# Kernel optimization log

Hardware: AMD Instinct MI355X
Metric: run time of the kernel (lower is better)

## Reference

```python
import jax, jax.numpy as jnp
import numpy as np

D = 512      # units / model dim
H = 8        # num_heads
K = 512      # key_dim (= units in this module)
B = 8
T = 512      # decoder length
S = 512      # encoder length
EPS = 1e-3   # Keras LayerNormalization default epsilon


def _layernorm(x, g, b):
    mu = jnp.mean(x, axis=-1, keepdims=True)
    var = jnp.mean(jnp.square(x - mu), axis=-1, keepdims=True)
    return (x - mu) * jax.lax.rsqrt(var + EPS) * g + b


def _mha(q_in, kv_in, wq, bq, wk, bk, wv, bv, wo, bo, causal):
    # q_in: [B,Tq,D], kv_in: [B,Tk,D]; wq/wk/wv: [D,H,K]; wo: [H,K,D]
    q = jnp.einsum('btd,dhk->bthk', q_in, wq) + bq
    k = jnp.einsum('bsd,dhk->bshk', kv_in, wk) + bk
    v = jnp.einsum('bsd,dhk->bshk', kv_in, wv) + bv
    scores = jnp.einsum('bqhk,bshk->bhqs', q, k) / jnp.sqrt(jnp.float32(K))
    if causal:
        Tq, Tk = q.shape[1], k.shape[1]
        mask = jnp.tril(jnp.ones((Tq, Tk), dtype=bool))
        scores = jnp.where(mask[None, None], scores, jnp.finfo(scores.dtype).min)
    attn = jax.nn.softmax(scores, axis=-1)
    out = jnp.einsum('bhqs,bshk->bqhk', attn, v)
    return jnp.einsum('bqhk,hkd->bqd', out, wo) + bo


def setup_inputs() -> dict:
    key = jax.random.key(0)
    ks = jax.random.split(key, 32)
    sc = 0.02
    d = {
        'in_seq': jax.random.normal(ks[0], (B, S, D), jnp.float32),
        'out_seq': jax.random.normal(ks[1], (B, T, D), jnp.float32),
    }
    i = 2
    for pfx in ('sa', 'ca'):
        d[pfx + '_wq'] = jax.random.normal(ks[i], (D, H, K)) * sc; i += 1
        d[pfx + '_bq'] = jnp.zeros((H, K))
        d[pfx + '_wk'] = jax.random.normal(ks[i], (D, H, K)) * sc; i += 1
        d[pfx + '_bk'] = jnp.zeros((H, K))
        d[pfx + '_wv'] = jax.random.normal(ks[i], (D, H, K)) * sc; i += 1
        d[pfx + '_bv'] = jnp.zeros((H, K))
        d[pfx + '_wo'] = jax.random.normal(ks[i], (H, K, D)) * sc; i += 1
        d[pfx + '_bo'] = jnp.zeros((D,))
        d[pfx + '_lng'] = jnp.ones((D,))
        d[pfx + '_lnb'] = jnp.zeros((D,))
    d['ff_w1'] = jax.random.normal(ks[i], (D, 2 * D)) * sc; i += 1
    d['ff_b1'] = jnp.zeros((2 * D,))
    d['ff_w2'] = jax.random.normal(ks[i], (2 * D, D)) * sc; i += 1
    d['ff_b2'] = jnp.zeros((D,))
    d['ff_lng'] = jnp.ones((D,))
    d['ff_lnb'] = jnp.zeros((D,))
    return d


def reference(in_seq, out_seq,
              sa_wq, sa_bq, sa_wk, sa_bk, sa_wv, sa_bv, sa_wo, sa_bo, sa_lng, sa_lnb,
              ca_wq, ca_bq, ca_wk, ca_bk, ca_wv, ca_bv, ca_wo, ca_bo, ca_lng, ca_lnb,
              ff_w1, ff_b1, ff_w2, ff_b2, ff_lng, ff_lnb):
    # causal self-attention + add + LN
    x = out_seq
    a = _mha(x, x, sa_wq, sa_bq, sa_wk, sa_bk, sa_wv, sa_bv, sa_wo, sa_bo, causal=True)
    x = _layernorm(x + a, sa_lng, sa_lnb)
    # cross-attention + add + LN
    a = _mha(x, in_seq, ca_wq, ca_bq, ca_wk, ca_bk, ca_wv, ca_bv, ca_wo, ca_bo, causal=False)
    x = _layernorm(x + a, ca_lng, ca_lnb)
    # FFN: Dense(2D, gelu) -> Dense(D) (dropout inactive at inference) + add + LN
    h = jax.nn.gelu(x @ ff_w1 + ff_b1, approximate=False)
    x = _layernorm(x + (h @ ff_w2 + ff_b2), ff_lng, ff_lnb)
    return x
```

## Files before the change

### kernel.cpp

```cpp
#include <hip/hip_runtime.h>
#include <math.h>

#define DEV __device__ __forceinline__

typedef __bf16 bf16x8 __attribute__((ext_vector_type(8)));
typedef float f32x4 __attribute__((ext_vector_type(4)));
typedef unsigned short u16x8 __attribute__((ext_vector_type(8)));

typedef const __attribute__((address_space(1))) void gv_t;
typedef __attribute__((address_space(3))) void lv_t;

DEV unsigned short f2bf(float f){
  unsigned int u = __float_as_uint(f);
  u += 0x7fffu + ((u >> 16) & 1u);
  return (unsigned short)(u >> 16);
}
DEV float bf2f(unsigned short u){ return __uint_as_float((unsigned)u << 16); }

DEV void gload16(const void* g, void* l){
  __builtin_amdgcn_global_load_lds((gv_t*)g, (lv_t*)l, 16, 0, 0);
}

DEV void xcd_decode(int& bx, int& by, int& bz){
  const int gx = gridDim.x, gy = gridDim.y;
  const int nwg = gx * gy * gridDim.z;
  int lin = blockIdx.x + gx*(blockIdx.y + gy*blockIdx.z);
  if ((nwg & 7) == 0) lin = (lin & 7)*(nwg >> 3) + (lin >> 3);
  bx = lin % gx; const int t = lin / gx;
  by = t % gy;  bz = t / gy;
}

struct Proj3 {
  const unsigned short* A[3];
  const unsigned short* B[3];
  unsigned short*       C[3];
  const float*          bias[3];
};

__global__ __launch_bounds__(512, 2)
void qkv256(Proj3 pr)
{
  __shared__ unsigned short Ab[2][2][8192];
  __shared__ unsigned short Bb[2][2][8192];

  int bxi, byi, bzi; xcd_decode(bxi, byi, bzi);
  const int m0 = byi*256, n0 = bxi*256;
  const unsigned short* A = pr.A[bzi];
  const unsigned short* B = pr.B[bzi];
  unsigned short*       C = pr.C[bzi];
  const float*       bias = pr.bias[bzi];

  const int tid = threadIdx.x, lane = tid & 63, w = tid >> 6;
  const int wr = w >> 2, wc = w & 3;
  const int l15 = lane & 15, l4 = lane >> 4;

  const int r8  = tid >> 3;
  const int sc8 = ((tid & 7) ^ (r8 & 7)) * 8;

  auto stageA = [&](int buf, int half, int kt){
    #pragma unroll
    for (int j = 0; j < 2; j++){
      const int lr = j*64 + r8;
      gload16(A + (size_t)(m0 + half*128 + lr)*512 + kt + sc8,
              &Ab[buf][half][j*4096 + tid*8]);
    }
  };
  auto stageB = [&](int buf, int half, int kt){
    #pragma unroll
    for (int j = 0; j < 2; j++){
      const int lr = j*64 + r8;
      gload16(B + (size_t)(n0 + half*128 + lr)*512 + kt + sc8,
              &Bb[buf][half][j*4096 + tid*8]);
    }
  };

  f32x4 acc[8][4] = {};

  stageB(0,0,0); stageB(0,1,0);
  stageA(0,0,0); stageA(0,1,0);
  stageA(1,0,64); stageA(1,1,64);
  stageB(1,0,64); stageB(1,1,64);
  asm volatile("s_waitcnt vmcnt(8)" ::: "memory");
  __builtin_amdgcn_s_barrier();
  __builtin_amdgcn_sched_barrier(0);

  const int nt = 8;
  for (int Q = 0; Q < nt; Q++){
    const int cur = Q & 1;
    if (Q > 0){
      if (Q + 1 < nt) asm volatile("s_waitcnt vmcnt(4)" ::: "memory");
      else            asm volatile("s_waitcnt vmcnt(0)" ::: "memory");
      __builtin_amdgcn_s_barrier();
      __builtin_amdgcn_sched_barrier(0);
    }
    bf16x8 bfr[4][2];
    #pragma unroll
    for (int s = 0; s < 4; s++){
      if (s == 0){
        #pragma unroll
        for (int fc = 0; fc < 4; fc++){
          const int R = wc*64 + fc*16 + l15;
          const int hb = R >> 7, lr = R & 127;
          #pragma unroll
          for (int kc = 0; kc < 2; kc++){
            const int cc = (kc*32 + l4*8) ^ ((lr & 7) * 8);
            bfr[fc][kc] = *(const bf16x8*)&Bb[cur][hb][lr*64 + cc];
          }
        }
      }
      bf16x8 ar[2][2];
      #pragma unroll
      for (int f = 0; f < 2; f++){
        const int lr = (s*2 + f)*16 + l15;
        #pragma unroll
        for (int kc = 0; kc < 2; kc++){
          const int cc = (kc*32 + l4*8) ^ ((lr & 7) * 8);
          ar[f][kc] = *(const bf16x8*)&Ab[cur][wr][lr*64 + cc];
        }
      }
      if (s == 0 && Q >= 1 && Q + 1 < nt) stageA(cur ^ 1, 0, (Q+1)*64);
      if (s == 1 && Q >= 1 && Q + 1 < nt) stageA(cur ^ 1, 1, (Q+1)*64);
      if (s == 2 && Q + 2 < nt)           stageB(cur,     0, (Q+2)*64);
      if (s == 3 && Q + 2 < nt)           stageB(cur,     1, (Q+2)*64);

      asm volatile("s_waitcnt lgkmcnt(0)" ::: "memory");
      __builtin_amdgcn_sched_barrier(0);
      __builtin_amdgcn_s_setprio(1);
      #pragma unroll
      for (int f = 0; f < 2; f++)
        #pragma unroll
        for (int fc = 0; fc < 4; fc++)
          #pragma unroll
          for (int kc = 0; kc < 2; kc++)
            acc[s*2+f][fc] = __builtin_amdgcn_mfma_f32_16x16x32_bf16(
                ar[f][kc], bfr[fc][kc], acc[s*2+f][fc], 0, 0, 0);
      __builtin_amdgcn_s_setprio(0);
      __builtin_amdgcn_s_barrier();
      __builtin_amdgcn_sched_barrier(0);
    }
  }

  if (bzi != 2){
    #pragma unroll
    for (int fr = 0; fr < 8; fr++){
      const int mb = m0 + wr*128 + fr*16 + l4*4;
      #pragma unroll
      for (int fc = 0; fc < 4; fc++){
        const int n = n0 + wc*64 + fc*16 + l15;
        const float bv = bias[n];
        #pragma unroll
        for (int r = 0; r < 4; r++)
          C[(size_t)(mb + r)*4096 + n] = f2bf(acc[fr][fc][r] + bv);
      }
    }
  } else {
    unsigned short* vt = C + ((size_t)((n0 >> 9)*8 + (m0 >> 9)))*262144;
    #pragma unroll
    for (int fr = 0; fr < 8; fr++){
      const int mb = m0 + wr*128 + fr*16 + l4*4;
      #pragma unroll
      for (int fc = 0; fc < 4; fc++){
        const int nl = (n0 & 256) + wc*64 + fc*16 + l15;
        #pragma unroll
        for (int r = 0; r < 4; r++){
          const int m = mb + r;
          const float bv = bias[m];
          vt[(size_t)((m0 & 256) + (m - m0))*512 + nl] = f2bf(acc[fr][fc][r] + bv);
        }
      }
    }
  }
}

template<int CMODE, int CSK>
__global__ __launch_bounds__(512, 2)
void gemm256(const unsigned short* __restrict__ A, const unsigned short* __restrict__ B,
             void* __restrict__ C, const float* __restrict__ bias,
             int M, int N, int K, int lda, int ldb, int ldc,
             size_t aOffH, size_t aOffB, size_t bOffH, size_t bOffB,
             size_t cOffH, size_t cOffB)
{
  __shared__ unsigned short Ab[2][2][8192];
  __shared__ unsigned short Bb[2][2][8192];

  int bxi, byi, bzi; xcd_decode(bxi, byi, bzi);
  const int m0 = byi*256, n0 = bxi*256;
  if (CSK == 1 && n0 > m0 + 255) return;

  const int z = bzi, bb = z >> 3, hh = z & 7;
  A += (size_t)bb*aOffB + (size_t)hh*aOffH;
  B += (size_t)bb*bOffB + (size_t)hh*bOffH;
  const size_t coff = (size_t)bb*cOffB + (size_t)hh*cOffH;

  const int tid = threadIdx.x, lane = tid & 63, w = tid >> 6;
  const int wr = w >> 2, wc = w & 3;
  const int l15 = lane & 15, l4 = lane >> 4;

  int Keff = K;
  if (CSK == 2) Keff = (m0 + 256 < K) ? (m0 + 256) : K;
  const int nt = Keff >> 6;

  const int r8  = tid >> 3;
  const int sc8 = ((tid & 7) ^ (r8 & 7)) * 8;

  auto stageA = [&](int buf, int half, int kt){
    #pragma unroll
    for (int j = 0; j < 2; j++){
      const int lr = j*64 + r8;
      gload16(A + (size_t)(m0 + half*128 + lr)*lda + kt + sc8,
              &Ab[buf][half][j*4096 + tid*8]);
    }
  };
  auto stageB = [&](int buf, int half, int kt){
    #pragma unroll
    for (int j = 0; j < 2; j++){
      const int lr = j*64 + r8;
      gload16(B + (size_t)(n0 + half*128 + lr)*ldb + kt + sc8,
              &Bb[buf][half][j*4096 + tid*8]);
    }
  };

  f32x4 acc[8][4] = {};

  stageB(0,0,0); stageB(0,1,0);
  stageA(0,0,0); stageA(0,1,0);
  if (nt > 1){
    stageA(1,0,64); stageA(1,1,64);
    stageB(1,0,64); stageB(1,1,64);
    asm volatile("s_waitcnt vmcnt(8)" ::: "memory");
  } else {
    asm volatile("s_waitcnt vmcnt(0)" ::: "memory");
  }
  __builtin_amdgcn_s_barrier();
  __builtin_amdgcn_sched_barrier(0);

  for (int Q = 0; Q < nt; Q++){
    const int cur = Q & 1;
    if (Q > 0){
      if (Q + 1 < nt) asm volatile("s_waitcnt vmcnt(4)" ::: "memory");
      else            asm volatile("s_waitcnt vmcnt(0)" ::: "memory");
      __builtin_amdgcn_s_barrier();
      __builtin_amdgcn_sched_barrier(0);
    }
    bf16x8 bfr[4][2];
    #pragma unroll
    for (int s = 0; s < 4; s++){
      if (s == 0){
        #pragma unroll
        for (int fc = 0; fc < 4; fc++){
          const int R = wc*64 + fc*16 + l15;
          const int hb = R >> 7, lr = R & 127;
          #pragma unroll
          for (int kc = 0; kc < 2; kc++){
            const int cc = (kc*32 + l4*8) ^ ((lr & 7) * 8);
            bfr[fc][kc] = *(const bf16x8*)&Bb[cur][hb][lr*64 + cc];
          }
        }
      }
      bf16x8 ar[2][2];
      #pragma unroll
      for (int f = 0; f < 2; f++){
        const int lr = (s*2 + f)*16 + l15;
        #pragma unroll
        for (int kc = 0; kc < 2; kc++){
          const int cc = (kc*32 + l4*8) ^ ((lr & 7) * 8);
          ar[f][kc] = *(const bf16x8*)&Ab[cur][wr][lr*64 + cc];
        }
      }
      if (s == 0 && Q >= 1 && Q + 1 < nt) stageA(cur ^ 1, 0, (Q+1)*64);
      if (s == 1 && Q >= 1 && Q + 1 < nt) stageA(cur ^ 1, 1, (Q+1)*64);
      if (s == 2 && Q + 2 < nt)           stageB(cur,     0, (Q+2)*64);
      if (s == 3 && Q + 2 < nt)           stageB(cur,     1, (Q+2)*64);

      asm volatile("s_waitcnt lgkmcnt(0)" ::: "memory");
      __builtin_amdgcn_sched_barrier(0);
      __builtin_amdgcn_s_setprio(1);
      #pragma unroll
      for (int f = 0; f < 2; f++)
        #pragma unroll
        for (int fc = 0; fc < 4; fc++)
          #pragma unroll
          for (int kc = 0; kc < 2; kc++)
            acc[s*2+f][fc] = __builtin_amdgcn_mfma_f32_16x16x32_bf16(
                ar[f][kc], bfr[fc][kc], acc[s*2+f][fc], 0, 0, 0);
      __builtin_amdgcn_s_setprio(0);
      __builtin_amdgcn_s_barrier();
      __builtin_amdgcn_sched_barrier(0);
    }
  }

  #pragma unroll
  for (int fr = 0; fr < 8; fr++){
    const int mb = m0 + wr*128 + fr*16 + l4*4;
    #pragma unroll
    for (int fc = 0; fc < 4; fc++){
      const int n = n0 + wc*64 + fc*16 + l15;
      const float bv = bias ? bias[n] : 0.0f;
      #pragma unroll
      for (int r = 0; r < 4; r++){
        const float v = acc[fr][fc][r] + bv;
        if (CMODE == 0) ((float*)C)[coff + (size_t)(mb + r)*ldc + n] = v;
        else            ((unsigned short*)C)[coff + (size_t)(mb + r)*ldc + n] = f2bf(v);
      }
    }
  }
}

template<int CMODE>
__global__ __launch_bounds__(256, 2)
void gemm_bt(const unsigned short* __restrict__ A, const unsigned short* __restrict__ B,
             void* __restrict__ C, const float* __restrict__ bias,
             int M, int N, int K, int lda, int ldb, int ldc,
             size_t aOffZ, size_t bOffZ, size_t cOffZ)
{
  __shared__ unsigned short Ab[2][8192];
  __shared__ unsigned short Bb[2][8192];

  int bxi, byi, bzi; xcd_decode(bxi, byi, bzi);
  const int m0 = byi*128, n0 = bxi*128;
  A += (size_t)bzi*aOffZ;
  B += (size_t)bzi*bOffZ;
  const size_t coff = (size_t)bzi*cOffZ;

  const int tid = threadIdx.x, lane = tid & 63, w = tid >> 6;
  const int wr = w >> 1, wc = w & 1;
  const int l15 = lane & 15, l4 = lane >> 4;
  const int nt = K >> 6;

  const int r8  = tid >> 3;
  const int sc8 = ((tid & 7) ^ (r8 & 7)) * 8;

  auto stage = [&](int buf, int kt){
    #pragma unroll
    for (int j = 0; j < 4; j++){
      gload16(A + (size_t)(m0 + j*32 + r8)*lda + kt + sc8, &Ab[buf][j*2048 + tid*8]);
      gload16(B + (size_t)(n0 + j*32 + r8)*ldb + kt + sc8, &Bb[buf][j*2048 + tid*8]);
    }
  };

  f32x4 acc[4][4] = {};

  stage(0, 0);
  __syncthreads();
  for (int t = 0; t < nt; t++){
    const int cur = t & 1;
    if (t + 1 < nt) stage(cur ^ 1, (t+1)*64);

    bf16x8 af[4][2], bfr[4][2];
    #pragma unroll
    for (int i = 0; i < 4; i++){
      const int Ra = wr*64 + i*16 + l15;
      const int Rb = wc*64 + i*16 + l15;
      #pragma unroll
      for (int kc = 0; kc < 2; kc++){
        const int ca = (kc*32 + l4*8) ^ ((Ra & 7) * 8);
        const int cb = (kc*32 + l4*8) ^ ((Rb & 7) * 8);
        af[i][kc]  = *(const bf16x8*)&Ab[cur][Ra*64 + ca];
        bfr[i][kc] = *(const bf16x8*)&Bb[cur][Rb*64 + cb];
      }
    }
    #pragma unroll
    for (int i = 0; i < 4; i++)
      #pragma unroll
      for (int jj = 0; jj < 4; jj++)
        #pragma unroll
        for (int kc = 0; kc < 2; kc++)
          acc[i][jj] = __builtin_amdgcn_mfma_f32_16x16x32_bf16(
              af[i][kc], bfr[jj][kc], acc[i][jj], 0, 0, 0);
    __syncthreads();
  }

  #pragma unroll
  for (int i = 0; i < 4; i++){
    const int mbase = m0 + wr*64 + i*16 + l4*4;
    #pragma unroll
    for (int jj = 0; jj < 4; jj++){
      const int n = n0 + wc*64 + jj*16 + l15;
      const float bv = bias ? bias[n] : 0.0f;
      #pragma unroll
      for (int r = 0; r < 4; r++){
        const int m = mbase + r;
        float v = acc[i][jj][r] + bv;
        if (CMODE == 0){
          ((float*)C)[coff + (size_t)m*ldc + n] = v;
        } else if (CMODE == 1){
          ((unsigned short*)C)[coff + (size_t)m*ldc + n] = f2bf(v);
        } else {
          v = 0.5f * v * (1.0f + erff(v * 0.70710678118654752f));
          ((unsigned short*)C)[coff + (size_t)m*ldc + n] = f2bf(v);
        }
      }
    }
  }
}

__global__ __launch_bounds__(256)
void gelu_reduce2(const unsigned short* __restrict__ p, size_t pstride,
                  const float* __restrict__ bias, unsigned short* __restrict__ out)
{
  const size_t i = ((size_t)blockIdx.x*256 + threadIdx.x)*8;
  const int nb = (int)(i & 1023);
  u16x8 a = *(const u16x8*)(p + i);
  u16x8 b = *(const u16x8*)(p + pstride + i);
  u16x8 o;
  #pragma unroll
  for (int j = 0; j < 8; j++){
    float v = bf2f(a[j]) + bf2f(b[j]) + bias[nb + j];
    v = 0.5f * v * (1.0f + erff(v * 0.70710678118654752f));
    o[j] = f2bf(v);
  }
  *(u16x8*)(out + i) = o;
}

template<int CAUSAL>
__global__ __launch_bounds__(256)
void softmax_rows(unsigned short* __restrict__ scores)
{
  const int row  = blockIdx.x*4 + (threadIdx.x >> 6);
  const int lane = threadIdx.x & 63;
  const int q = row & 511;
  unsigned short* srow = scores + (size_t)row*512;
  u16x8 sv = *(const u16x8*)(srow + lane*8);
  float s[8]; float m = -1e30f;
  #pragma unroll
  for (int i = 0; i < 8; i++){
    const int col = lane*8 + i;
    float v = bf2f(sv[i]) * 0.044194173824159216f;
    if (CAUSAL && col > q) v = -1e30f;
    s[i] = v; m = fmaxf(m, v);
  }
  #pragma unroll
  for (int o = 32; o; o >>= 1) m = fmaxf(m, __shfl_xor(m, o));
  float p[8], sum = 0.f;
  #pragma unroll
  for (int i = 0; i < 8; i++){
    float e = __expf(s[i] - m);
    if (CAUSAL && (lane*8 + i) > q) e = 0.f;
    p[i] = e; sum += e;
  }
  #pragma unroll
  for (int o = 32; o; o >>= 1) sum += __shfl_xor(sum, o);
  const float inv = 1.0f / sum;
  u16x8 pv;
  #pragma unroll
  for (int i = 0; i < 8; i++) pv[i] = f2bf(p[i] * inv);
  *(u16x8*)(srow + lane*8) = pv;
}

template<int WRITE_BF, int ND, int BFP>
__global__ __launch_bounds__(256)
void ln_rows(const float* __restrict__ x, const void* __restrict__ dbase,
             size_t dstride, const float* __restrict__ bias,
             const float* __restrict__ g, const float* __restrict__ bta,
             float* __restrict__ xo, unsigned short* __restrict__ xb)
{
  const int row = blockIdx.x*4 + (threadIdx.x >> 6);
  const int lane = threadIdx.x & 63;
  const float* xr = x + (size_t)row*512;
  float v[8];
  #pragma unroll
  for (int i = 0; i < 8; i++){
    const int c = lane*8 + i;
    v[i] = xr[c] + (bias ? bias[c] : 0.0f);
  }
  #pragma unroll
  for (int p = 0; p < ND; p++){
    if (BFP){
      const unsigned short* db = (const unsigned short*)dbase;
      u16x8 dv = *(const u16x8*)(db + p*dstride + (size_t)row*512 + lane*8);
      #pragma unroll
      for (int i = 0; i < 8; i++) v[i] += bf2f(dv[i]);
    } else {
      const float* db = (const float*)dbase;
      #pragma unroll
      for (int i = 0; i < 8; i++) v[i] += db[p*dstride + (size_t)row*512 + lane*8 + i];
    }
  }
  float sum = 0.f;
  #pragma unroll
  for (int i = 0; i < 8; i++) sum += v[i];
  #pragma unroll
  for (int o = 32; o; o >>= 1) sum += __shfl_xor(sum, o);
  const float mean = sum * (1.0f/512.0f);
  float s2 = 0.f;
  #pragma unroll
  for (int i = 0; i < 8; i++){ const float t = v[i] - mean; s2 += t*t; }
  #pragma unroll
  for (int o = 32; o; o >>= 1) s2 += __shfl_xor(s2, o);
  const float inv = rsqrtf(s2 * (1.0f/512.0f) + 1e-3f);
  #pragma unroll
  for (int i = 0; i < 8; i++){
    const int c = lane*8 + i;
    const float y = (v[i] - mean)*inv*g[c] + bta[c];
    xo[(size_t)row*512 + c] = y;
    if (WRITE_BF) xb[(size_t)row*512 + c] = f2bf(y);
  }
}

struct Cast2 { const float* s[2]; unsigned short* d[2]; };

__global__ __launch_bounds__(256)
void cast_bf16_k2(Cast2 a, int n)
{
  const int z = blockIdx.y;
  const int i = (blockIdx.x*256 + threadIdx.x)*4;
  if (i < n){
    const float4 v = *(const float4*)(a.s[z] + i);
    uint2 o;
    o.x = (unsigned)f2bf(v.x) | ((unsigned)f2bf(v.y) << 16);
    o.y = (unsigned)f2bf(v.z) | ((unsigned)f2bf(v.w) << 16);
    *(uint2*)(a.d[z] + i) = o;
  }
}

struct TC8 { const float* s[8]; unsigned short* d[8]; };

__global__ __launch_bounds__(256)
void transpose_cast8(TC8 a, int R, int C)
{
  __shared__ float tile[32][33];
  const int z = blockIdx.z;
  const float* src = a.s[z];
  unsigned short* dst = a.d[z];
  const int bx = blockIdx.x*32, by = blockIdx.y*32;
  const int tx = threadIdx.x & 31, ty = threadIdx.x >> 5;
  #pragma unroll
  for (int i = 0; i < 32; i += 8) tile[ty + i][tx] = src[(size_t)(by + ty + i)*C + bx + tx];
  __syncthreads();
  #pragma unroll
  for (int i = 0; i < 32; i += 8) dst[(size_t)(bx + ty + i)*R + by + tx] = f2bf(tile[tx][ty + i]);
}

extern "C" void kernel_launch(void* const* d_in, const int* in_sizes, int n_in,
                              void* d_out, int out_size, void* d_ws, size_t ws_size,
                              hipStream_t stream)
{
  (void)in_sizes; (void)n_in; (void)out_size; (void)ws_size;

  const float* in_seq  = (const float*)d_in[0];
  const float* out_seq = (const float*)d_in[1];
  const float* sa_wq = (const float*)d_in[2];  const float* sa_bq = (const float*)d_in[3];
  const float* sa_wk = (const float*)d_in[4];  const float* sa_bk = (const float*)d_in[5];
  const float* sa_wv = (const float*)d_in[6];  const float* sa_bv = (const float*)d_in[7];
  const float* sa_wo = (const float*)d_in[8];  const float* sa_bo = (const float*)d_in[9];
  const float* sa_lng = (const float*)d_in[10]; const float* sa_lnb = (const float*)d_in[11];
  const float* ca_wq = (const float*)d_in[12]; const float* ca_bq = (const float*)d_in[13];
  const float* ca_wk = (const float*)d_in[14]; const float* ca_bk = (const float*)d_in[15];
  const float* ca_wv = (const float*)d_in[16]; const float* ca_bv = (const float*)d_in[17];
  const float* ca_wo = (const float*)d_in[18]; const float* ca_bo = (const float*)d_in[19];
  const float* ca_lng = (const float*)d_in[20]; const float* ca_lnb = (const float*)d_in[21];
  const float* ff_w1 = (const float*)d_in[22]; const float* ff_b1 = (const float*)d_in[23];
  const float* ff_w2 = (const float*)d_in[24]; const float* ff_b2 = (const float*)d_in[25];
  const float* ff_lng = (const float*)d_in[26]; const float* ff_lnb = (const float*)d_in[27];

  char* ws = (char*)d_ws;
  size_t off = 0;
  auto alloc = [&](size_t bytes){ char* p = ws + off; off += (bytes + 255) & ~(size_t)255; return p; };

  unsigned short* wT[8];
  for (int i = 0; i < 8; i++) wT[i] = (unsigned short*)alloc(4096ULL*512*2);
  unsigned short* w1T  = (unsigned short*)alloc(1024ULL*512*2);
  unsigned short* w2T  = (unsigned short*)alloc(512ULL*1024*2);
  unsigned short* xbf  = (unsigned short*)alloc(4096ULL*512*2);
  unsigned short* inbf = (unsigned short*)alloc(4096ULL*512*2);
  unsigned short* qb   = (unsigned short*)alloc(4096ULL*4096*2);
  unsigned short* kb   = (unsigned short*)alloc(4096ULL*4096*2);
  unsigned short* vT   = (unsigned short*)alloc(64ULL*512*512*2);
  unsigned short* scb  = (unsigned short*)alloc(64ULL*512*512*2);
  float*          xcur = (float*)alloc(4096ULL*512*4);

  unsigned short* part = scb;
  const size_t PART_STRIDE = 2097152;
  const size_t FF1_STRIDE = 4194304;

  Cast2 c2{{out_seq, in_seq}, {xbf, inbf}};
  cast_bf16_k2<<<dim3(2048,2), 256, 0, stream>>>(c2, 4096*512);

  TC8 tqkv{{sa_wq, sa_wk, sa_wv, ca_wq, ca_wk, ca_wv, nullptr, nullptr},
           {wT[0], wT[1], wT[2], wT[4], wT[5], wT[6], nullptr, nullptr}};
  transpose_cast8<<<dim3(128,16,6), 256, 0, stream>>>(tqkv, 512, 4096);
  TC8 two{{sa_wo, ca_wo, nullptr,nullptr,nullptr,nullptr,nullptr,nullptr},
          {wT[3], wT[7], nullptr,nullptr,nullptr,nullptr,nullptr,nullptr}};
  transpose_cast8<<<dim3(16,128,2), 256, 0, stream>>>(two, 4096, 512);
  TC8 tw1{{ff_w1, nullptr,nullptr,nullptr,nullptr,nullptr,nullptr,nullptr},
          {w1T, nullptr,nullptr,nullptr,nullptr,nullptr,nullptr,nullptr}};
  transpose_cast8<<<dim3(32,16,1), 256, 0, stream>>>(tw1, 512, 1024);
  TC8 tw2{{ff_w2, nullptr,nullptr,nullptr,nullptr,nullptr,nullptr,nullptr},
          {w2T, nullptr,nullptr,nullptr,nullptr,nullptr,nullptr,nullptr}};
  transpose_cast8<<<dim3(16,32,1), 256, 0, stream>>>(tw2, 1024, 512);

  #define G256(MODE, CSK, Apt, Bpt, Cpt, BIAS, M, N, K, LDA, LDB, LDC, Z, aH, aB, bH, bB, cH, cB) \
    gemm256<MODE, CSK><<<dim3((N)/256,(M)/256,(Z)), 512, 0, stream>>>( \
      (const unsigned short*)(Apt), (const unsigned short*)(Bpt), (void*)(Cpt), BIAS, \
      M, N, K, LDA, LDB, LDC, aH, aB, bH, bB, cH, cB)

  Proj3 saP{{xbf, xbf, wT[2]}, {wT[0], wT[1], xbf}, {qb, kb, vT}, {sa_bq, sa_bk, sa_bv}};
  qkv256<<<dim3(16,16,3), 512, 0, stream>>>(saP);
  G256(1, 1, qb, kb, scb, nullptr, 512, 512, 512, 4096, 4096, 512, 64,
       512, 2097152, 512, 2097152, 262144, 2097152);
  softmax_rows<1><<<8192, 256, 0, stream>>>(scb);
  G256(1, 2, scb, vT, kb, nullptr, 512, 512, 512, 512, 512, 4096, 64,
       262144, 2097152, 262144, 2097152, 512, 2097152);
  G256(1, 0, kb, wT[3], part, nullptr, 4096, 512, 512, 4096, 4096, 512, 8,
       512, 0, 512, 0, PART_STRIDE, 0);
  ln_rows<1, 8, 1><<<1024, 256, 0, stream>>>(out_seq, part, PART_STRIDE,
                                             sa_bo, sa_lng, sa_lnb, xcur, xbf);

  Proj3 caP{{xbf, inbf, wT[6]}, {wT[4], wT[5], inbf}, {qb, kb, vT}, {ca_bq, ca_bk, ca_bv}};
  qkv256<<<dim3(16,16,3), 512, 0, stream>>>(caP);
  G256(1, 0, qb, kb, scb, nullptr, 512, 512, 512, 4096, 4096, 512, 64,
       512, 2097152, 512, 2097152, 262144, 2097152);
  softmax_rows<0><<<8192, 256, 0, stream>>>(scb);
  G256(1, 0, scb, vT, kb, nullptr, 512, 512, 512, 512, 512, 4096, 64,
       262144, 2097152, 262144, 2097152, 512, 2097152);
  G256(1, 0, kb, wT[7], part, nullptr, 4096, 512, 512, 4096, 4096, 512, 8,
       512, 0, 512, 0, PART_STRIDE, 0);
  ln_rows<1, 8, 1><<<1024, 256, 0, stream>>>(xcur, part, PART_STRIDE,
                                             ca_bo, ca_lng, ca_lnb, xcur, xbf);

  gemm_bt<1><<<dim3(8,32,2), 256, 0, stream>>>(
      xbf, w1T, (void*)part, nullptr, 4096, 1024, 256, 512, 512, 1024,
      256, 256, FF1_STRIDE);
  gelu_reduce2<<<2048, 256, 0, stream>>>(part, FF1_STRIDE, ff_b1, qb);
  G256(1, 0, qb, w2T, part, nullptr, 4096, 512, 128, 1024, 1024, 512, 8,
       128, 0, 128, 0, PART_STRIDE, 0);
  ln_rows<0, 8, 1><<<1024, 256, 0, stream>>>(xcur, part, PART_STRIDE,
                                             ff_b2, ff_lng, ff_lnb, (float*)d_out, nullptr);

  #undef G256
}
```

Before: 417.1 us.

## Merge weight transpose launches, drop fp32 residual buffer, skip masked causal loads

Folds the four weight transpose-cast launches into one flat-grid kernel that uses a per-tile table. The fp32 residual buffer xcur is removed, so layernorm now reads and writes only the bf16 activation, which cuts memory traffic and lowers the residual to bf16 precision. The causal softmax no longer loads score chunks that lie entirely above the diagonal. The bf16 residual adds rounding error to the layer output.

```diff
diff --git a/kernel.cpp b/kernel.cpp
--- a/kernel.cpp
+++ b/kernel.cpp
@@ -420,7 +420,8 @@
   const int lane = threadIdx.x & 63;
   const int q = row & 511;
   unsigned short* srow = scores + (size_t)row*512;
-  u16x8 sv = *(const u16x8*)(srow + lane*8);
+  u16x8 sv = {};
+  if (!CAUSAL || lane*8 <= q) sv = *(const u16x8*)(srow + lane*8);
   float s[8]; float m = -1e30f;
   #pragma unroll
   for (int i = 0; i < 8; i++){
@@ -447,34 +448,32 @@
   *(u16x8*)(srow + lane*8) = pv;
 }
 
-template<int WRITE_BF, int ND, int BFP>
+template<int XF32, int OUTF32, int ND>
 __global__ __launch_bounds__(256)
-void ln_rows(const float* __restrict__ x, const void* __restrict__ dbase,
+void ln_rows(const void* __restrict__ x, const unsigned short* __restrict__ dbase,
              size_t dstride, const float* __restrict__ bias,
              const float* __restrict__ g, const float* __restrict__ bta,
-             float* __restrict__ xo, unsigned short* __restrict__ xb)
+             void* __restrict__ out)
 {
   const int row = blockIdx.x*4 + (threadIdx.x >> 6);
   const int lane = threadIdx.x & 63;
-  const float* xr = x + (size_t)row*512;
   float v[8];
-  #pragma unroll
-  for (int i = 0; i < 8; i++){
-    const int c = lane*8 + i;
-    v[i] = xr[c] + (bias ? bias[c] : 0.0f);
-  }
+  if (XF32){
+    const float* xr = (const float*)x + (size_t)row*512 + lane*8;
+    #pragma unroll
+    for (int i = 0; i < 8; i++) v[i] = xr[i];
+  } else {
+    u16x8 xv = *(const u16x8*)((const unsigned short*)x + (size_t)row*512 + lane*8);
+    #pragma unroll
+    for (int i = 0; i < 8; i++) v[i] = bf2f(xv[i]);
+  }
+  #pragma unroll
+  for (int i = 0; i < 8; i++) v[i] += bias ? bias[lane*8 + i] : 0.0f;
   #pragma unroll
   for (int p = 0; p < ND; p++){
-    if (BFP){
-      const unsigned short* db = (const unsigned short*)dbase;
-      u16x8 dv = *(const u16x8*)(db + p*dstride + (size_t)row*512 + lane*8);
-      #pragma unroll
-      for (int i = 0; i < 8; i++) v[i] += bf2f(dv[i]);
-    } else {
-      const float* db = (const float*)dbase;
-      #pragma unroll
-      for (int i = 0; i < 8; i++) v[i] += db[p*dstride + (size_t)row*512 + lane*8 + i];
-    }
+    u16x8 dv = *(const u16x8*)(dbase + p*dstride + (size_t)row*512 + lane*8);
+    #pragma unroll
+    for (int i = 0; i < 8; i++) v[i] += bf2f(dv[i]);
   }
   float sum = 0.f;
   #pragma unroll
@@ -488,12 +487,21 @@
   #pragma unroll
   for (int o = 32; o; o >>= 1) s2 += __shfl_xor(s2, o);
   const float inv = rsqrtf(s2 * (1.0f/512.0f) + 1e-3f);
-  #pragma unroll
-  for (int i = 0; i < 8; i++){
-    const int c = lane*8 + i;
-    const float y = (v[i] - mean)*inv*g[c] + bta[c];
-    xo[(size_t)row*512 + c] = y;
-    if (WRITE_BF) xb[(size_t)row*512 + c] = f2bf(y);
+  if (OUTF32){
+    float* po = (float*)out + (size_t)row*512 + lane*8;
+    #pragma unroll
+    for (int i = 0; i < 8; i++){
+      const int c = lane*8 + i;
+      po[i] = (v[i] - mean)*inv*g[c] + bta[c];
+    }
+  } else {
+    u16x8 ov;
+    #pragma unroll
+    for (int i = 0; i < 8; i++){
+      const int c = lane*8 + i;
+      ov[i] = f2bf((v[i] - mean)*inv*g[c] + bta[c]);
+    }
+    *(u16x8*)((unsigned short*)out + (size_t)row*512 + lane*8) = ov;
   }
 }
 
@@ -513,16 +521,25 @@
   }
 }
 
-struct TC8 { const float* s[8]; unsigned short* d[8]; };
+struct TCA {
+  const float* s[10]; unsigned short* d[10];
+  int Cc[10]; int Rr[10]; int cw[10];
+  int start[11];
+};
 
 __global__ __launch_bounds__(256)
-void transpose_cast8(TC8 a, int R, int C)
+void transpose_cast_all(TCA a)
 {
   __shared__ float tile[32][33];
-  const int z = blockIdx.z;
-  const float* src = a.s[z];
-  unsigned short* dst = a.d[z];
-  const int bx = blockIdx.x*32, by = blockIdx.y*32;
+  const int bid = blockIdx.x;
+  int t = 0;
+  #pragma unroll
+  for (int k = 0; k < 9; k++) if (bid >= a.start[k+1]) t = k+1;
+  const float* src = a.s[t];
+  unsigned short* dst = a.d[t];
+  const int C = a.Cc[t], R = a.Rr[t];
+  const int local = bid - a.start[t];
+  const int bx = (local % a.cw[t])*32, by = (local / a.cw[t])*32;
   const int tx = threadIdx.x & 31, ty = threadIdx.x >> 5;
   #pragma unroll
   for (int i = 0; i < 32; i += 8) tile[ty + i][tx] = src[(size_t)(by + ty + i)*C + bx + tx];
@@ -567,7 +584,6 @@
   unsigned short* kb   = (unsigned short*)alloc(4096ULL*4096*2);
   unsigned short* vT   = (unsigned short*)alloc(64ULL*512*512*2);
   unsigned short* scb  = (unsigned short*)alloc(64ULL*512*512*2);
-  float*          xcur = (float*)alloc(4096ULL*512*4);
 
   unsigned short* part = scb;
   const size_t PART_STRIDE = 2097152;
@@ -576,18 +592,20 @@
   Cast2 c2{{out_seq, in_seq}, {xbf, inbf}};
   cast_bf16_k2<<<dim3(2048,2), 256, 0, stream>>>(c2, 4096*512);
 
-  TC8 tqkv{{sa_wq, sa_wk, sa_wv, ca_wq, ca_wk, ca_wv, nullptr, nullptr},
-           {wT[0], wT[1], wT[2], wT[4], wT[5], wT[6], nullptr, nullptr}};
-  transpose_cast8<<<dim3(128,16,6), 256, 0, stream>>>(tqkv, 512, 4096);
-  TC8 two{{sa_wo, ca_wo, nullptr,nullptr,nullptr,nullptr,nullptr,nullptr},
-          {wT[3], wT[7], nullptr,nullptr,nullptr,nullptr,nullptr,nullptr}};
-  transpose_cast8<<<dim3(16,128,2), 256, 0, stream>>>(two, 4096, 512);
-  TC8 tw1{{ff_w1, nullptr,nullptr,nullptr,nullptr,nullptr,nullptr,nullptr},
-          {w1T, nullptr,nullptr,nullptr,nullptr,nullptr,nullptr,nullptr}};
-  transpose_cast8<<<dim3(32,16,1), 256, 0, stream>>>(tw1, 512, 1024);
-  TC8 tw2{{ff_w2, nullptr,nullptr,nullptr,nullptr,nullptr,nullptr,nullptr},
-          {w2T, nullptr,nullptr,nullptr,nullptr,nullptr,nullptr,nullptr}};
-  transpose_cast8<<<dim3(16,32,1), 256, 0, stream>>>(tw2, 1024, 512);
+  TCA ta;
+  const float* srcs[10] = {sa_wq, sa_wk, sa_wv, ca_wq, ca_wk, ca_wv, sa_wo, ca_wo, ff_w1, ff_w2};
+  unsigned short* dsts[10] = {wT[0], wT[1], wT[2], wT[4], wT[5], wT[6], wT[3], wT[7], w1T, w2T};
+  const int Rs[10] = {512,512,512,512,512,512, 4096,4096, 512, 1024};
+  const int Cs[10] = {4096,4096,4096,4096,4096,4096, 512,512, 1024, 512};
+  int acc_ = 0;
+  for (int t = 0; t < 10; t++){
+    ta.s[t] = srcs[t]; ta.d[t] = dsts[t];
+    ta.Rr[t] = Rs[t]; ta.Cc[t] = Cs[t]; ta.cw[t] = Cs[t]/32;
+    ta.start[t] = acc_;
+    acc_ += (Cs[t]/32)*(Rs[t]/32);
+  }
+  ta.start[10] = acc_;
+  transpose_cast_all<<<acc_, 256, 0, stream>>>(ta);
 
   #define G256(MODE, CSK, Apt, Bpt, Cpt, BIAS, M, N, K, LDA, LDB, LDC, Z, aH, aB, bH, bB, cH, cB) \
     gemm256<MODE, CSK><<<dim3((N)/256,(M)/256,(Z)), 512, 0, stream>>>( \
@@ -603,8 +621,8 @@
        262144, 2097152, 262144, 2097152, 512, 2097152);
   G256(1, 0, kb, wT[3], part, nullptr, 4096, 512, 512, 4096, 4096, 512, 8,
        512, 0, 512, 0, PART_STRIDE, 0);
-  ln_rows<1, 8, 1><<<1024, 256, 0, stream>>>(out_seq, part, PART_STRIDE,
-                                             sa_bo, sa_lng, sa_lnb, xcur, xbf);
+  ln_rows<1, 0, 8><<<1024, 256, 0, stream>>>(out_seq, part, PART_STRIDE,
+                                             sa_bo, sa_lng, sa_lnb, xbf);
 
   Proj3 caP{{xbf, inbf, wT[6]}, {wT[4], wT[5], inbf}, {qb, kb, vT}, {ca_bq, ca_bk, ca_bv}};
   qkv256<<<dim3(16,16,3), 512, 0, stream>>>(caP);
@@ -615,8 +633,8 @@
        262144, 2097152, 262144, 2097152, 512, 2097152);
   G256(1, 0, kb, wT[7], part, nullptr, 4096, 512, 512, 4096, 4096, 512, 8,
        512, 0, 512, 0, PART_STRIDE, 0);
-  ln_rows<1, 8, 1><<<1024, 256, 0, stream>>>(xcur, part, PART_STRIDE,
-                                             ca_bo, ca_lng, ca_lnb, xcur, xbf);
+  ln_rows<0, 0, 8><<<1024, 256, 0, stream>>>(xbf, part, PART_STRIDE,
+                                             ca_bo, ca_lng, ca_lnb, xbf);
 
   gemm_bt<1><<<dim3(8,32,2), 256, 0, stream>>>(
       xbf, w1T, (void*)part, nullptr, 4096, 1024, 256, 512, 512, 1024,
@@ -624,8 +642,8 @@
   gelu_reduce2<<<2048, 256, 0, stream>>>(part, FF1_STRIDE, ff_b1, qb);
   G256(1, 0, qb, w2T, part, nullptr, 4096, 512, 128, 1024, 1024, 512, 8,
        128, 0, 128, 0, PART_STRIDE, 0);
-  ln_rows<0, 8, 1><<<1024, 256, 0, stream>>>(xcur, part, PART_STRIDE,
-                                             ff_b2, ff_lng, ff_lnb, (float*)d_out, nullptr);
+  ln_rows<0, 1, 8><<<1024, 256, 0, stream>>>(xbf, part, PART_STRIDE,
+                                             ff_b2, ff_lng, ff_lnb, (float*)d_out);
 
   #undef G256
 }
```

After: 412.1 us. Within noise of the previous version (-1.2%).
